# Kernel optimization log

Measured on AMD Instinct MI355X. Metric: run time of the kernel, lower is better.

The kernel has to match this reference:

```python
import jax, jax.numpy as jnp
import numpy as np

N = 50000
E = 1600000
IN_DIM = 128
HID = 32
HEADS = 4
OUT = 32
NEG_SLOPE = 0.2


def gat_conv(h, src, dst, W, al, ar, b, n_heads, d_out):
    # h: [N, F_in]; W: [F_in, H*D]; al/ar: [H, D]; b: [H*D]
    n = h.shape[0]
    z = (h @ W).reshape(n, n_heads, d_out)            # [N,H,D]
    el = (z * al[None]).sum(-1)                        # [N,H]
    er = (z * ar[None]).sum(-1)                        # [N,H]
    e = el[src] + er[dst]                              # [E,H]
    e = jnp.where(e > 0, e, NEG_SLOPE * e)             # leaky_relu(0.2)
    # edge softmax grouped by destination node
    m = jax.ops.segment_max(e, dst, num_segments=n)    # [N,H]
    ex = jnp.exp(e - m[dst])                           # [E,H]
    s = jax.ops.segment_sum(ex, dst, num_segments=n)   # [N,H]
    alpha = ex / s[dst]                                # [E,H]
    msg = alpha[:, :, None] * z[src]                   # [E,H,D]
    out = jax.ops.segment_sum(msg, dst, num_segments=n)  # [N,H,D]
    return out + b.reshape(1, n_heads, d_out)


def setup_inputs() -> dict:
    key = jax.random.key(0)
    ks = jax.random.split(key, 12)
    h = jax.random.normal(ks[0], (N, IN_DIM), dtype=jnp.float32)
    src = jax.random.randint(ks[1], (E,), 0, N, dtype=jnp.int32)
    dst = jax.random.randint(ks[2], (E,), 0, N, dtype=jnp.int32)
    s1 = 1.0 / np.sqrt(IN_DIM)
    W1 = jax.random.uniform(ks[3], (IN_DIM, HEADS * HID), jnp.float32, -s1, s1)
    al1 = jax.random.normal(ks[4], (HEADS, HID), jnp.float32) * 0.1
    ar1 = jax.random.normal(ks[5], (HEADS, HID), jnp.float32) * 0.1
    b1 = jnp.zeros((HEADS * HID,), jnp.float32)
    f2 = HEADS * HID
    s2 = 1.0 / np.sqrt(f2)
    W2 = jax.random.uniform(ks[6], (f2, OUT), jnp.float32, -s2, s2)
    al2 = jax.random.normal(ks[7], (1, OUT), jnp.float32) * 0.1
    ar2 = jax.random.normal(ks[8], (1, OUT), jnp.float32) * 0.1
    b2 = jnp.zeros((OUT,), jnp.float32)
    return {"h": h, "src": src, "dst": dst, "W1": W1, "al1": al1, "ar1": ar1,
            "b1": b1, "W2": W2, "al2": al2, "ar2": ar2, "b2": b2}


def reference(h, src, dst, W1, al1, ar1, b1, W2, al2, ar2, b2):
    x = gat_conv(h, src, dst, W1, al1, ar1, b1, HEADS, HID)  # [N,H,D]
    x = x.reshape(N, HEADS * HID)                             # flatten(1)
    x = jax.nn.elu(x)                                         # act
    y = gat_conv(x, src, dst, W2, al2, ar2, b2, 1, OUT)       # [N,1,OUT]
    return y.squeeze(1)                                        # [N,OUT]
```

## Files before the change

kernel.cpp:

```cpp
#include <hip/hip_runtime.h>
#include <hip/hip_fp16.h>

#define NN 50000
#define NEG_SLOPE 0.2f
#define BSHIFT 9
#define BNODES (1 << BSHIFT)
#define NBUCK ((NN + BNODES - 1) >> BSHIFT)
#define BCAP 18432

typedef _Float16 f16x4 __attribute__((ext_vector_type(4)));
typedef _Float16 f16x8 __attribute__((ext_vector_type(8)));
typedef float    f32x4 __attribute__((ext_vector_type(4)));

__global__ void zero_kernel(unsigned* bucket_cursor) {
    int i = threadIdx.x;
    if (i < NBUCK) bucket_cursor[i] = (unsigned)(i * BCAP);
}

__global__ __launch_bounds__(1024) void bucketA(
        const int* __restrict__ src, const int* __restrict__ dst,
        unsigned* __restrict__ bucket_cursor, int2* __restrict__ ebuf, int E) {
    __shared__ unsigned hist[NBUCK];
    int tid = threadIdx.x;
    if (tid < NBUCK) hist[tid] = 0u;
    __syncthreads();
    int e = blockIdx.x * 1024 + tid;
    int s = 0, d = 0, b = 0;
    bool valid = e < E;
    if (valid) {
        s = src[e]; d = dst[e]; b = d >> BSHIFT;
        atomicAdd(&hist[b], 1u);
    }
    __syncthreads();
    if (tid < NBUCK) {
        unsigned c = hist[tid];
        hist[tid] = c ? atomicAdd(&bucket_cursor[tid], c) : 0u;
    }
    __syncthreads();
    if (valid) {
        unsigned slot = atomicAdd(&hist[b], 1u);
        ebuf[slot] = make_int2(s, d);
    }
}

__global__ __launch_bounds__(256) void gemm1_mfma(
        const float* __restrict__ h, const float* __restrict__ W1,
        const float* __restrict__ al1, const float* __restrict__ ar1,
        __half* __restrict__ z1h, float* __restrict__ el1, float* __restrict__ er1, int N) {
    __shared__ alignas(16) __half hA[64 * 128];
    __shared__ alignas(16) __half Bt[128 * 128];
    int tid = threadIdx.x;
    int lane = tid & 63, w = tid >> 6;
    int row0 = blockIdx.x * 64;
    int nrow = min(64, N - row0);

    for (int idx = tid; idx < 64 * 32; idx += 256) {
        int row = idx >> 5, kq = idx & 31;
        float4 v = (row < nrow) ? ((const float4*)(h + (size_t)(row0 + row) * 128))[kq]
                                : make_float4(0.f, 0.f, 0.f, 0.f);
        f16x4 hv;
        hv[0] = (_Float16)v.x; hv[1] = (_Float16)v.y;
        hv[2] = (_Float16)v.z; hv[3] = (_Float16)v.w;
        int off = row * 256 + ((kq * 8) ^ ((row & 15) << 4));
        *(f16x4*)((char*)hA + off) = hv;
    }
    {
        int col = tid & 127, kg = (tid >> 7) & 1;
        #pragma unroll
        for (int it = 0; it < 8; ++it) {
            int k0 = it * 16 + kg * 8;
            f16x8 wv;
            #pragma unroll
            for (int i = 0; i < 8; ++i)
                wv[i] = (_Float16)W1[(size_t)(k0 + i) * 128 + col];
            int off = col * 256 + ((k0 * 2) ^ ((col & 15) << 4));
            *(f16x8*)((char*)Bt + off) = wv;
        }
    }
    __syncthreads();

    f32x4 acc[8];
    #pragma unroll
    for (int ct = 0; ct < 8; ++ct) acc[ct] = (f32x4){0.f, 0.f, 0.f, 0.f};

    int arow = w * 16 + (lane & 15);
    int kbyte_lane = ((lane >> 4) * 8) * 2;
    #pragma unroll
    for (int ks = 0; ks < 4; ++ks) {
        int kb = ks * 64 + kbyte_lane;
        f16x8 a = *(const f16x8*)((const char*)hA + arow * 256 + (kb ^ ((arow & 15) << 4)));
        #pragma unroll
        for (int ct = 0; ct < 8; ++ct) {
            int col = ct * 16 + (lane & 15);
            f16x8 b = *(const f16x8*)((const char*)Bt + col * 256 + (kb ^ ((col & 15) << 4)));
            acc[ct] = __builtin_amdgcn_mfma_f32_16x16x32_f16(a, b, acc[ct], 0, 0, 0);
        }
    }

    int lrow = (lane >> 4) * 4;
    #pragma unroll
    for (int ct = 0; ct < 8; ++ct) {
        int col = ct * 16 + (lane & 15);
        #pragma unroll
        for (int r = 0; r < 4; ++r) {
            int rl = w * 16 + lrow + r;
            if (rl < nrow)
                z1h[(size_t)(row0 + rl) * 128 + col] = __float2half(acc[ct][r]);
        }
    }
    #pragma unroll
    for (int hh = 0; hh < 4; ++hh) {
        int c0 = hh * 32 + (lane & 15);
        float a_l0 = al1[c0], a_l1 = al1[c0 + 16];
        float a_r0 = ar1[c0], a_r1 = ar1[c0 + 16];
        #pragma unroll
        for (int r = 0; r < 4; ++r) {
            float v0 = acc[2 * hh][r], v1 = acc[2 * hh + 1][r];
            float pl = v0 * a_l0 + v1 * a_l1;
            float pr = v0 * a_r0 + v1 * a_r1;
            #pragma unroll
            for (int o = 8; o; o >>= 1) {
                pl += __shfl_xor(pl, o, 16);
                pr += __shfl_xor(pr, o, 16);
            }
            int rl = w * 16 + lrow + r;
            if ((lane & 15) == 0 && rl < nrow) {
                el1[(row0 + rl) * 4 + hh] = pl;
                er1[(row0 + rl) * 4 + hh] = pr;
            }
        }
    }
}

__global__ __launch_bounds__(1024) void scatterC(
        const int2* __restrict__ ebuf, const unsigned* __restrict__ bucket_cursor,
        const float* __restrict__ el1, const float* __restrict__ er1,
        unsigned* __restrict__ off, int* __restrict__ src_sorted,
        uint2* __restrict__ alpha1p, int N, int E) {
    __shared__ unsigned hist[BNODES], nodeoff[BNODES], wsum[8], bsz[128];
    __shared__ float4 er_s[BNODES];
    int b = blockIdx.x, tid = threadIdx.x;
    int base = b << BSHIFT;
    unsigned rs = (unsigned)(b * BCAP), re = bucket_cursor[b];
    const float4* el1v = (const float4*)el1;
    const float4* er1v = (const float4*)er1;

    if (tid < 128) bsz[tid] = (tid < NBUCK) ? bucket_cursor[tid] - (unsigned)(tid * BCAP) : 0u;
    if (tid < BNODES) {
        hist[tid] = 0u;
        int n = base + tid;
        er_s[tid] = (n < N) ? er1v[n] : make_float4(0.f, 0.f, 0.f, 0.f);
    }
    __syncthreads();
    if (tid == 0) {
        unsigned r = 0;
        for (int t = 0; t < NBUCK; ++t) { unsigned c = bsz[t]; bsz[t] = r; r += c; }
        if (b == 0) off[N] = (unsigned)E;
    }
    __syncthreads();
    unsigned boff = bsz[b];

    for (unsigned i = rs + tid; i < re; i += 1024)
        atomicAdd(&hist[ebuf[i].y - base], 1u);
    __syncthreads();
    unsigned v = 0, x = 0;
    int lane = tid & 63, wv = tid >> 6;
    if (tid < BNODES) {
        v = hist[tid]; x = v;
        #pragma unroll
        for (int o = 1; o < 64; o <<= 1) {
            unsigned n = __shfl_up(x, o, 64);
            if (lane >= o) x += n;
        }
        if (lane == 63) wsum[wv] = x;
    }
    __syncthreads();
    if (tid == 0) {
        unsigned r = 0;
        #pragma unroll
        for (int k = 0; k < 8; ++k) { unsigned t = wsum[k]; wsum[k] = r; r += t; }
    }
    __syncthreads();
    if (tid < BNODES) {
        unsigned exoff = x - v + wsum[wv] + boff;
        nodeoff[tid] = exoff;
        if (base + tid < N) off[base + tid] = exoff;
        hist[tid] = 0u;
    }
    __syncthreads();
    for (unsigned i = rs + tid; i < re; i += 1024) {
        int2 ed = ebuf[i];
        int ln = ed.y - base;
        unsigned r = atomicAdd(&hist[ln], 1u);
        unsigned p = nodeoff[ln] + r;
        src_sorted[p] = ed.x;
        float4 el = el1v[ed.x];
        float4 er = er_s[ln];
        float v0 = el.x + er.x; v0 = v0 > 0.f ? v0 : NEG_SLOPE * v0;
        float v1 = el.y + er.y; v1 = v1 > 0.f ? v1 : NEG_SLOPE * v1;
        float v2 = el.z + er.z; v2 = v2 > 0.f ? v2 : NEG_SLOPE * v2;
        float v3 = el.w + er.w; v3 = v3 > 0.f ? v3 : NEG_SLOPE * v3;
        union { __half2 h2[2]; uint2 u; } pk;
        pk.h2[0] = __floats2half2_rn(__expf(v0), __expf(v1));
        pk.h2[1] = __floats2half2_rn(__expf(v2), __expf(v3));
        alpha1p[p] = pk.u;
    }
}

__global__ __launch_bounds__(256) void agg1_spmm(
        const int* __restrict__ src_sorted, const unsigned* __restrict__ off,
        const __half* __restrict__ alpha1h, const __half* __restrict__ z1h,
        const float* __restrict__ b1, __half* __restrict__ x) {
    int tid = threadIdx.x, lane = tid & 63, w = tid >> 6;
    int node = blockIdx.x * 4 + w;
    int start = (int)off[node], end = (int)off[node + 1];
    int g = lane >> 4, l16 = lane & 15, head = l16 >> 2, j = l16 & 3;

    float acc[8];
    #pragma unroll
    for (int jj = 0; jj < 8; ++jj) acc[jj] = 0.f;
    float sloc = 0.f;
    int endm1 = end - 1;
    for (int base = start; base < end; base += 32) {
        #pragma unroll
        for (int t = 0; t < 8; ++t) {
            int i = base + 4 * t + g;
            int ic = min(i, endm1);
            int s = src_sorted[ic];
            float a = __half2float(alpha1h[ic * 4 + head]);
            a = (i < end) ? a : 0.f;
            sloc += (j == 0) ? a : 0.f;
            float4 r = *(const float4*)(z1h + ((size_t)s << 7) + l16 * 8);
            const __half* zh = (const __half*)&r;
            #pragma unroll
            for (int k = 0; k < 8; ++k)
                acc[k] = fmaf(__half2float(zh[k]), a, acc[k]);
        }
    }
    #pragma unroll
    for (int jj = 0; jj < 8; ++jj) {
        acc[jj] += __shfl_xor(acc[jj], 16, 64);
        acc[jj] += __shfl_xor(acc[jj], 32, 64);
    }
    sloc += __shfl_xor(sloc, 1, 64);
    sloc += __shfl_xor(sloc, 2, 64);
    sloc += __shfl_xor(sloc, 16, 64);
    sloc += __shfl_xor(sloc, 32, 64);
    float inv = sloc > 0.f ? 1.f / sloc : 0.f;

    if (g == 0) {
        float xv[8];
        #pragma unroll
        for (int jj = 0; jj < 8; ++jj) {
            float t = acc[jj] * inv + b1[l16 * 8 + jj];
            xv[jj] = t > 0.f ? t : (__expf(t) - 1.f);
        }
        union { __half2 h2[4]; uint4 u; } pk;
        #pragma unroll
        for (int k = 0; k < 4; ++k) pk.h2[k] = __floats2half2_rn(xv[2 * k], xv[2 * k + 1]);
        *(uint4*)(x + ((size_t)node << 7) + l16 * 8) = pk.u;
    }
}

__global__ __launch_bounds__(256) void gemm2el_kernel(
        const __half* __restrict__ x, const float* __restrict__ W2,
        const float* __restrict__ al2, const float* __restrict__ ar2,
        __half* __restrict__ z2h, float* __restrict__ el2, float* __restrict__ er2, int N) {
    __shared__ __half xsh[64][136];
    __shared__ float W2T[32][132];
    int tid = threadIdx.x;
    int row0 = blockIdx.x * 64;
    int nrow = min(64, N - row0);

    for (int idx = tid; idx < nrow * 16; idx += 256) {
        int r = idx >> 4, kq = idx & 15;
        float4 v = ((const float4*)(x + (size_t)(row0 + r) * 128))[kq];
        *(float4*)&xsh[r][kq * 8] = v;
    }
    for (int idx = tid; idx < 4096; idx += 256) {
        int k = idx >> 5, c = idx & 31;
        W2T[c][k] = W2[idx];
    }
    __syncthreads();

    int gc = tid & 15, gr = tid >> 4;
    float acc[4][2];
    #pragma unroll
    for (int j = 0; j < 4; ++j) { acc[j][0] = 0.f; acc[j][1] = 0.f; }

    for (int p = 0; p < 32; ++p) {
        float4 w0 = *(const float4*)&W2T[gc][p * 4];
        float4 w1 = *(const float4*)&W2T[gc + 16][p * 4];
        #pragma unroll
        for (int j = 0; j < 4; ++j) {
            const __half* xr = &xsh[gr * 4 + j][p * 4];
            float x0 = __half2float(xr[0]), x1 = __half2float(xr[1]);
            float x2 = __half2float(xr[2]), x3 = __half2float(xr[3]);
            acc[j][0] = fmaf(x0, w0.x, fmaf(x1, w0.y, fmaf(x2, w0.z, fmaf(x3, w0.w, acc[j][0]))));
            acc[j][1] = fmaf(x0, w1.x, fmaf(x1, w1.y, fmaf(x2, w1.z, fmaf(x3, w1.w, acc[j][1]))));
        }
    }

    float al0 = al2[gc], al1v = al2[gc + 16];
    float ar0 = ar2[gc], ar1v = ar2[gc + 16];
    #pragma unroll
    for (int j = 0; j < 4; ++j) {
        int r = gr * 4 + j;
        int node = row0 + r;
        bool live = r < nrow;
        if (live) {
            z2h[(size_t)node * 32 + gc]      = __float2half(acc[j][0]);
            z2h[(size_t)node * 32 + gc + 16] = __float2half(acc[j][1]);
        }
        float pl = acc[j][0] * al0 + acc[j][1] * al1v;
        float pr = acc[j][0] * ar0 + acc[j][1] * ar1v;
        #pragma unroll
        for (int o = 8; o; o >>= 1) {
            pl += __shfl_xor(pl, o, 16);
            pr += __shfl_xor(pr, o, 16);
        }
        if (live && gc == 0) { el2[node] = pl; er2[node] = pr; }
    }
}

__global__ __launch_bounds__(256) void agg2_fused(
        const int* __restrict__ src_sorted, const unsigned* __restrict__ off,
        const float* __restrict__ el2, const float* __restrict__ er2,
        const __half* __restrict__ z2h, const float* __restrict__ b2,
        float* __restrict__ out) {
    int tid = threadIdx.x, lane = tid & 63;
    int node = blockIdx.x * 4 + (tid >> 6);
    int start = (int)off[node], end = (int)off[node + 1];
    float er_d = er2[node];

    int g = lane >> 2, l4 = lane & 3;
    float acc[8];
    #pragma unroll
    for (int jj = 0; jj < 8; ++jj) acc[jj] = 0.f;
    float sloc = 0.f;
    int endm1 = end - 1;
    for (int base = start; base < end; base += 64) {
        #pragma unroll
        for (int t = 0; t < 4; ++t) {
            int i = base + 16 * t + g;
            int ic = min(i, endm1);
            int s = src_sorted[ic];
            float v = el2[s] + er_d;
            v = v > 0.f ? v : NEG_SLOPE * v;
            float ex = __expf(v);
            ex = (i < end) ? ex : 0.f;
            sloc += (l4 == 0) ? ex : 0.f;
            float4 r = *(const float4*)(z2h + ((size_t)s << 5) + l4 * 8);
            const __half* zh = (const __half*)&r;
            #pragma unroll
            for (int k = 0; k < 8; ++k)
                acc[k] = fmaf(__half2float(zh[k]), ex, acc[k]);
        }
    }
    #pragma unroll
    for (int jj = 0; jj < 8; ++jj) {
        acc[jj] += __shfl_xor(acc[jj], 4, 64);
        acc[jj] += __shfl_xor(acc[jj], 8, 64);
        acc[jj] += __shfl_xor(acc[jj], 16, 64);
        acc[jj] += __shfl_xor(acc[jj], 32, 64);
    }
    #pragma unroll
    for (int o = 32; o; o >>= 1) sloc += __shfl_xor(sloc, o, 64);
    float inv = sloc > 0.f ? 1.f / sloc : 0.f;
    if (g == 0) {
        #pragma unroll
        for (int jj = 0; jj < 8; ++jj)
            out[(size_t)node * 32 + l4 * 8 + jj] = acc[jj] * inv + b2[l4 * 8 + jj];
    }
}

extern "C" void kernel_launch(void* const* d_in, const int* in_sizes, int n_in,
                              void* d_out, int out_size, void* d_ws, size_t ws_size,
                              hipStream_t stream) {
    const float* h   = (const float*)d_in[0];
    const int*   src = (const int*)d_in[1];
    const int*   dst = (const int*)d_in[2];
    const float* W1  = (const float*)d_in[3];
    const float* al1 = (const float*)d_in[4];
    const float* ar1 = (const float*)d_in[5];
    const float* b1  = (const float*)d_in[6];
    const float* W2  = (const float*)d_in[7];
    const float* al2 = (const float*)d_in[8];
    const float* ar2 = (const float*)d_in[9];
    const float* b2  = (const float*)d_in[10];
    float* out = (float*)d_out;
    const int N = NN;
    const int E = in_sizes[1];

    char* w = (char*)d_ws;
    __half* z1h       = (__half*)w;   w += (size_t)N * 128 * 2;
    __half* z2h       = (__half*)w;   w += (size_t)N * 32 * 2;
    __half* xh        = (__half*)w;   w += (size_t)N * 128 * 2;
    int2*  ebuf       = (int2*)w;     w += (size_t)NBUCK * BCAP * 8;
    uint2* alpha1p    = (uint2*)w;    w += (size_t)E * 8;
    int*   src_sorted = (int*)w;      w += (size_t)E * 4;
    float* el1        = (float*)w;    w += (size_t)N * 4 * 4;
    float* er1        = (float*)w;    w += (size_t)N * 4 * 4;
    float* el2        = (float*)w;    w += (size_t)N * 4;
    float* er2        = (float*)w;    w += (size_t)N * 4;
    unsigned* off     = (unsigned*)w; w += (size_t)(N + 16) * 4;
    unsigned* bucket_cursor = (unsigned*)w; w += 128 * 4;

    zero_kernel<<<1, 128, 0, stream>>>(bucket_cursor);
    bucketA<<<(E + 1023) / 1024, 1024, 0, stream>>>(src, dst, bucket_cursor, ebuf, E);
    gemm1_mfma<<<(N + 63) / 64, 256, 0, stream>>>(h, W1, al1, ar1, z1h, el1, er1, N);
    scatterC<<<NBUCK, 1024, 0, stream>>>(ebuf, bucket_cursor, el1, er1,
                                         off, src_sorted, alpha1p, N, E);
    agg1_spmm<<<N / 4, 256, 0, stream>>>(src_sorted, off, (const __half*)alpha1p, z1h, b1, xh);
    gemm2el_kernel<<<(N + 63) / 64, 256, 0, stream>>>(xh, W2, al2, ar2, z2h, el2, er2, N);
    agg2_fused<<<N / 4, 256, 0, stream>>>(src_sorted, off, el2, er2, z2h, b2, out);
}
```

Baseline: 293.0 us.

## Tune GEMM1 tiling, pad edge arrays, use nontemporal loads and cheaper softmax sums

```diff
diff --git a/kernel.cpp b/kernel.cpp
--- a/kernel.cpp
+++ b/kernel.cpp
@@ -11,10 +11,12 @@
 typedef _Float16 f16x4 __attribute__((ext_vector_type(4)));
 typedef _Float16 f16x8 __attribute__((ext_vector_type(8)));
 typedef float    f32x4 __attribute__((ext_vector_type(4)));
-
-__global__ void zero_kernel(unsigned* bucket_cursor) {
+typedef unsigned int u32x4 __attribute__((ext_vector_type(4)));
+
+__global__ void zero_kernel(unsigned* bucket_cursor, int* src_sorted_pad) {
     int i = threadIdx.x;
     if (i < NBUCK) bucket_cursor[i] = (unsigned)(i * BCAP);
+    if (i < 64) src_sorted_pad[i] = 0;
 }
 
 __global__ __launch_bounds__(1024) void bucketA(
@@ -43,18 +45,18 @@
     }
 }
 
-__global__ __launch_bounds__(256) void gemm1_mfma(
+__global__ __launch_bounds__(512) void gemm1_mfma(
         const float* __restrict__ h, const float* __restrict__ W1,
         const float* __restrict__ al1, const float* __restrict__ ar1,
         __half* __restrict__ z1h, float* __restrict__ el1, float* __restrict__ er1, int N) {
-    __shared__ alignas(16) __half hA[64 * 128];
+    __shared__ alignas(16) __half hA[128 * 128];
     __shared__ alignas(16) __half Bt[128 * 128];
     int tid = threadIdx.x;
     int lane = tid & 63, w = tid >> 6;
-    int row0 = blockIdx.x * 64;
-    int nrow = min(64, N - row0);
-
-    for (int idx = tid; idx < 64 * 32; idx += 256) {
+    int row0 = blockIdx.x * 128;
+    int nrow = min(128, N - row0);
+
+    for (int idx = tid; idx < 128 * 32; idx += 512) {
         int row = idx >> 5, kq = idx & 31;
         float4 v = (row < nrow) ? ((const float4*)(h + (size_t)(row0 + row) * 128))[kq]
                                 : make_float4(0.f, 0.f, 0.f, 0.f);
@@ -65,10 +67,10 @@
         *(f16x4*)((char*)hA + off) = hv;
     }
     {
-        int col = tid & 127, kg = (tid >> 7) & 1;
-        #pragma unroll
-        for (int it = 0; it < 8; ++it) {
-            int k0 = it * 16 + kg * 8;
+        int col = tid & 127, kg = tid >> 7;
+        #pragma unroll
+        for (int it = 0; it < 4; ++it) {
+            int k0 = it * 32 + kg * 8;
             f16x8 wv;
             #pragma unroll
             for (int i = 0; i < 8; ++i)
@@ -196,10 +198,10 @@
         src_sorted[p] = ed.x;
         float4 el = el1v[ed.x];
         float4 er = er_s[ln];
-        float v0 = el.x + er.x; v0 = v0 > 0.f ? v0 : NEG_SLOPE * v0;
-        float v1 = el.y + er.y; v1 = v1 > 0.f ? v1 : NEG_SLOPE * v1;
-        float v2 = el.z + er.z; v2 = v2 > 0.f ? v2 : NEG_SLOPE * v2;
-        float v3 = el.w + er.w; v3 = v3 > 0.f ? v3 : NEG_SLOPE * v3;
+        float v0 = el.x + er.x; v0 = fmaxf(v0, NEG_SLOPE * v0);
+        float v1 = el.y + er.y; v1 = fmaxf(v1, NEG_SLOPE * v1);
+        float v2 = el.z + er.z; v2 = fmaxf(v2, NEG_SLOPE * v2);
+        float v3 = el.w + er.w; v3 = fmaxf(v3, NEG_SLOPE * v3);
         union { __half2 h2[2]; uint2 u; } pk;
         pk.h2[0] = __floats2half2_rn(__expf(v0), __expf(v1));
         pk.h2[1] = __floats2half2_rn(__expf(v2), __expf(v3));
@@ -214,23 +216,25 @@
     int tid = threadIdx.x, lane = tid & 63, w = tid >> 6;
     int node = blockIdx.x * 4 + w;
     int start = (int)off[node], end = (int)off[node + 1];
-    int g = lane >> 4, l16 = lane & 15, head = l16 >> 2, j = l16 & 3;
+    int g = lane >> 4, l16 = lane & 15, head = l16 >> 2;
+    const char* zbase = (const char*)z1h + (unsigned)(l16 * 16);
+    const unsigned short* au = (const unsigned short*)alpha1h;
 
     float acc[8];
     #pragma unroll
     for (int jj = 0; jj < 8; ++jj) acc[jj] = 0.f;
     float sloc = 0.f;
-    int endm1 = end - 1;
     for (int base = start; base < end; base += 32) {
         #pragma unroll
         for (int t = 0; t < 8; ++t) {
             int i = base + 4 * t + g;
-            int ic = min(i, endm1);
-            int s = src_sorted[ic];
-            float a = __half2float(alpha1h[ic * 4 + head]);
+            int s = __builtin_nontemporal_load(src_sorted + i);
+            unsigned short us = __builtin_nontemporal_load(au + ((unsigned)i * 4u + head));
+            __half ah = *reinterpret_cast<__half*>(&us);
+            float a = __half2float(ah);
             a = (i < end) ? a : 0.f;
-            sloc += (j == 0) ? a : 0.f;
-            float4 r = *(const float4*)(z1h + ((size_t)s << 7) + l16 * 8);
+            sloc += a;
+            float4 r = *(const float4*)(zbase + ((unsigned)s << 8));
             const __half* zh = (const __half*)&r;
             #pragma unroll
             for (int k = 0; k < 8; ++k)
@@ -242,8 +246,6 @@
         acc[jj] += __shfl_xor(acc[jj], 16, 64);
         acc[jj] += __shfl_xor(acc[jj], 32, 64);
     }
-    sloc += __shfl_xor(sloc, 1, 64);
-    sloc += __shfl_xor(sloc, 2, 64);
     sloc += __shfl_xor(sloc, 16, 64);
     sloc += __shfl_xor(sloc, 32, 64);
     float inv = sloc > 0.f ? 1.f / sloc : 0.f;
@@ -255,10 +257,10 @@
             float t = acc[jj] * inv + b1[l16 * 8 + jj];
             xv[jj] = t > 0.f ? t : (__expf(t) - 1.f);
         }
-        union { __half2 h2[4]; uint4 u; } pk;
+        union { __half2 h2[4]; u32x4 u; } pk;
         #pragma unroll
         for (int k = 0; k < 4; ++k) pk.h2[k] = __floats2half2_rn(xv[2 * k], xv[2 * k + 1]);
-        *(uint4*)(x + ((size_t)node << 7) + l16 * 8) = pk.u;
+        __builtin_nontemporal_store(pk.u, (u32x4*)(x + ((size_t)node << 7) + l16 * 8));
     }
 }
 
@@ -334,23 +336,22 @@
     float er_d = er2[node];
 
     int g = lane >> 2, l4 = lane & 3;
+    const char* zbase = (const char*)z2h + (unsigned)(l4 * 16);
     float acc[8];
     #pragma unroll
     for (int jj = 0; jj < 8; ++jj) acc[jj] = 0.f;
     float sloc = 0.f;
-    int endm1 = end - 1;
     for (int base = start; base < end; base += 64) {
         #pragma unroll
         for (int t = 0; t < 4; ++t) {
             int i = base + 16 * t + g;
-            int ic = min(i, endm1);
-            int s = src_sorted[ic];
+            int s = __builtin_nontemporal_load(src_sorted + i);
             float v = el2[s] + er_d;
-            v = v > 0.f ? v : NEG_SLOPE * v;
+            v = fmaxf(v, NEG_SLOPE * v);
             float ex = __expf(v);
             ex = (i < end) ? ex : 0.f;
-            sloc += (l4 == 0) ? ex : 0.f;
-            float4 r = *(const float4*)(z2h + ((size_t)s << 5) + l4 * 8);
+            sloc += ex;
+            float4 r = *(const float4*)(zbase + ((unsigned)s << 6));
             const __half* zh = (const __half*)&r;
             #pragma unroll
             for (int k = 0; k < 8; ++k)
@@ -364,8 +365,10 @@
         acc[jj] += __shfl_xor(acc[jj], 16, 64);
         acc[jj] += __shfl_xor(acc[jj], 32, 64);
     }
-    #pragma unroll
-    for (int o = 32; o; o >>= 1) sloc += __shfl_xor(sloc, o, 64);
+    sloc += __shfl_xor(sloc, 4, 64);
+    sloc += __shfl_xor(sloc, 8, 64);
+    sloc += __shfl_xor(sloc, 16, 64);
+    sloc += __shfl_xor(sloc, 32, 64);
     float inv = sloc > 0.f ? 1.f / sloc : 0.f;
     if (g == 0) {
         #pragma unroll
@@ -397,8 +400,8 @@
     __half* z2h       = (__half*)w;   w += (size_t)N * 32 * 2;
     __half* xh        = (__half*)w;   w += (size_t)N * 128 * 2;
     int2*  ebuf       = (int2*)w;     w += (size_t)NBUCK * BCAP * 8;
-    uint2* alpha1p    = (uint2*)w;    w += (size_t)E * 8;
-    int*   src_sorted = (int*)w;      w += (size_t)E * 4;
+    uint2* alpha1p    = (uint2*)w;    w += ((size_t)E + 32) * 8;
+    int*   src_sorted = (int*)w;      w += ((size_t)E + 64) * 4;
     float* el1        = (float*)w;    w += (size_t)N * 4 * 4;
     float* er1        = (float*)w;    w += (size_t)N * 4 * 4;
     float* el2        = (float*)w;    w += (size_t)N * 4;
@@ -406,9 +409,9 @@
     unsigned* off     = (unsigned*)w; w += (size_t)(N + 16) * 4;
     unsigned* bucket_cursor = (unsigned*)w; w += 128 * 4;
 
-    zero_kernel<<<1, 128, 0, stream>>>(bucket_cursor);
+    zero_kernel<<<1, 128, 0, stream>>>(bucket_cursor, src_sorted + E);
     bucketA<<<(E + 1023) / 1024, 1024, 0, stream>>>(src, dst, bucket_cursor, ebuf, E);
-    gemm1_mfma<<<(N + 63) / 64, 256, 0, stream>>>(h, W1, al1, ar1, z1h, el1, er1, N);
+    gemm1_mfma<<<(N + 127) / 128, 512, 0, stream>>>(h, W1, al1, ar1, z1h, el1, er1, N);
     scatterC<<<NBUCK, 1024, 0, stream>>>(ebuf, bucket_cursor, el1, er1,
                                          off, src_sorted, alpha1p, N, E);
     agg1_spmm<<<N / 4, 256, 0, stream>>>(src_sorted, off, (const __half*)alpha1p, z1h, b1, xh);
```

Measured after the change: 300.3 us. +2.5%, slower.
